# Kernel tuning notes

Hardware: AMD Instinct MI355X
Metric: run time of the kernel (lower is better)

Reference implementation:

```python
import jax, jax.numpy as jnp
import numpy as np
import math

B, L, D_IN = 4, 8192, 64
H = 256          # d_model
N2 = 32          # d_state // 2 complex conjugate pairs (S4D)
NL = 4           # n_layers
D_OUT = 10


def setup_inputs() -> dict:
    key = jax.random.key(0)
    ks = jax.random.split(key, 16)
    x = jax.random.normal(ks[0], (B, L, D_IN), dtype=jnp.float32)
    # encoder Linear(d_input, d_model)
    enc_W = jax.random.normal(ks[1], (H, D_IN), dtype=jnp.float32) / np.sqrt(D_IN)
    enc_b = jnp.zeros((H,), dtype=jnp.float32)
    # per-layer S4D parameters (stacked over n_layers)
    log_dt = jax.random.uniform(ks[2], (NL, H), dtype=jnp.float32,
                                minval=math.log(1e-3), maxval=math.log(1e-1))
    log_A_re = jnp.full((NL, H, N2), math.log(0.5), dtype=jnp.float32)
    A_im = jnp.tile(math.pi * jnp.arange(N2, dtype=jnp.float32), (NL, H, 1))
    C_re = jax.random.normal(ks[3], (NL, H, N2), dtype=jnp.float32) * (0.5 ** 0.5)
    C_im = jax.random.normal(ks[4], (NL, H, N2), dtype=jnp.float32) * (0.5 ** 0.5)
    D = jax.random.normal(ks[5], (NL, H), dtype=jnp.float32)
    # S4 block output linear (H -> 2H) followed by GLU
    Wo = jax.random.normal(ks[6], (NL, 2 * H, H), dtype=jnp.float32) / np.sqrt(H)
    bo = jnp.zeros((NL, 2 * H), dtype=jnp.float32)
    # post-norm LayerNorm over d_model
    ln_w = jnp.ones((NL, H), dtype=jnp.float32)
    ln_b = jnp.zeros((NL, H), dtype=jnp.float32)
    # final decoder Linear(d_model, d_output)
    out_W = jax.random.normal(ks[7], (D_OUT, H), dtype=jnp.float32) / np.sqrt(H)
    out_b = jnp.zeros((D_OUT,), dtype=jnp.float32)
    return dict(x=x, enc_W=enc_W, enc_b=enc_b, log_dt=log_dt, log_A_re=log_A_re,
                A_im=A_im, C_re=C_re, C_im=C_im, D=D, Wo=Wo, bo=bo,
                ln_w=ln_w, ln_b=ln_b, out_W=out_W, out_b=out_b)


def _s4d_kernel(log_dt, log_A_re, A_im, C_re, C_im, L):
    # S4D-ZOH-ish (S4D-Lin) kernel: K[h,l] = 2 Re sum_n C~[h,n] exp(l*dt*A[h,n])
    dt = jnp.exp(log_dt)[:, None]                      # (H,1)
    A = -jnp.exp(log_A_re) + 1j * A_im                 # (H,N2)
    dtA = dt * A                                       # (H,N2)
    Ct = (C_re + 1j * C_im) * (jnp.exp(dtA) - 1.0) / A # (H,N2)
    t = jnp.arange(L, dtype=jnp.float32)
    V = jnp.exp(dtA[:, :, None] * t)                   # (H,N2,L) Vandermonde
    return 2.0 * jnp.einsum('hn,hnl->hl', Ct, V).real  # (H,L)


def reference(x, enc_W, enc_b, log_dt, log_A_re, A_im, C_re, C_im, D, Wo, bo,
              ln_w, ln_b, out_W, out_b):
    Bc, Lc, _ = x.shape
    h = x @ enc_W.T + enc_b          # (B,L,H)
    h = h.transpose(0, 2, 1)         # (B,H,L) (transposed layout)
    n_layers = log_dt.shape[0]
    for i in range(n_layers):
        K = _s4d_kernel(log_dt[i], log_A_re[i], A_im[i], C_re[i], C_im[i], Lc)
        # FFT convolution (causal, non-circular via 2L padding)
        Kf = jnp.fft.rfft(K, n=2 * Lc)                       # (H, L+1)
        hf = jnp.fft.rfft(h, n=2 * Lc)                       # (B,H,L+1)
        y = jnp.fft.irfft(hf * Kf, n=2 * Lc)[..., :Lc]
        y = y + D[i][:, None] * h                            # skip D*u
        y = jax.nn.gelu(y)
        # output linear (H -> 2H) + GLU, pointwise over length
        u = jnp.einsum('oh,bhl->bol', Wo[i], y) + bo[i][:, None]
        Hd = h.shape[1]
        z = u[:, :Hd] * jax.nn.sigmoid(u[:, Hd:])
        h = z + h                                            # residual
        # post-norm LayerNorm over channel (d_model) dim
        mu = h.mean(axis=1, keepdims=True)
        var = h.var(axis=1, keepdims=True)
        h = (h - mu) / jnp.sqrt(var + 1e-5) * ln_w[i][:, None] + ln_b[i][:, None]
    h = h.transpose(0, 2, 1)          # (B,L,H)
    return h @ out_W.T + out_b        # (B,L,d_output)
```

## Files before the change

### kernel.cpp

```cpp
#include <hip/hip_runtime.h>
#include <hip/hip_bf16.h>


constexpr int B_ = 4, L_ = 8192, DIN = 64, H_ = 256, N2_ = 32, NL_ = 4, DOUT = 10;
constexpr int LC = 64, CHK = L_ / LC;
constexpr int GCH = B_ * CHK;
constexpr int M_ = B_ * L_;

constexpr size_t OFF_H    = 0;
constexpr size_t OFF_WOB  = 8388608;
constexpr size_t OFF_PW   = 8650752;
constexpr size_t OFF_PCT  = 8716288;
constexpr size_t OFF_PWLC = 8781824;
constexpr size_t OFF_PZ   = 8847360;
constexpr size_t OFF_EWT  = 8912896;
constexpr size_t OFF_UCM  = 8929280;
constexpr size_t OFF_YCM  = 13123584;
constexpr size_t OFF_MT   = 21512192;
constexpr size_t OFF_MW   = 22036480;
constexpr size_t OFF_MV   = 22560768;

typedef short bf16x8 __attribute__((ext_vector_type(8)));
typedef short short8 __attribute__((ext_vector_type(8)));
typedef float f32x4  __attribute__((ext_vector_type(4)));
typedef int   int2v  __attribute__((ext_vector_type(2)));

__device__ __forceinline__ float b2f(short s) {
    union { float f; unsigned u; } c;
    c.u = ((unsigned)(unsigned short)s) << 16;
    return c.f;
}

__global__ __launch_bounds__(256) void k_params(
    const float* __restrict__ log_dt, const float* __restrict__ log_A_re,
    const float* __restrict__ A_im, const float* __restrict__ C_re,
    const float* __restrict__ C_im, float* __restrict__ ws)
{
    int idx = blockIdx.x * 256 + threadIdx.x;
    if (idx >= NL_ * H_ * N2_) return;
    int i  = idx / (H_ * N2_);
    int hh = (idx / N2_) % H_;
    float dt  = expf(log_dt[i * H_ + hh]);
    float Are = -expf(log_A_re[idx]);
    float Aim = A_im[idx];
    float zre = dt * Are, zim = dt * Aim;
    float er  = expf(zre);
    float wre = er * cosf(zim), wim = er * sinf(zim);
    float d   = Are * Are + Aim * Aim;
    float nre = wre - 1.f, nim = wim;
    float qre = (nre * Are + nim * Aim) / d;
    float qim = (nim * Are - nre * Aim) / d;
    float cr = C_re[idx], ci = C_im[idx];
    float ctre = cr * qre - ci * qim;
    float ctim = cr * qim + ci * qre;
    float er2 = expf(zre * (float)LC);
    float wlre = er2 * cosf(zim * (float)LC);
    float wlim = er2 * sinf(zim * (float)LC);
    ((float2*)(ws + OFF_PW))[idx]   = make_float2(wre, wim);
    ((float2*)(ws + OFF_PCT))[idx]  = make_float2(2.f * ctre, 2.f * ctim);
    ((float2*)(ws + OFF_PWLC))[idx] = make_float2(wlre, wlim);
    ((float2*)(ws + OFF_PZ))[idx]   = make_float2(zre, zim);
}

__global__ __launch_bounds__(256) void k_mats(const float* __restrict__ ws,
    int layer, __hip_bfloat16* __restrict__ mt, __hip_bfloat16* __restrict__ mw,
    __hip_bfloat16* __restrict__ mv)
{
    int h = blockIdx.x, tid = threadIdx.x;
    __shared__ float zre[32], zim[32], ctr[32], cti[32], kv[64];
    if (tid < 32) {
        float2 z = ((const float2*)(ws + OFF_PZ))[(size_t)layer*H_*N2_ + h*N2_ + tid];
        float2 c = ((const float2*)(ws + OFF_PCT))[(size_t)layer*H_*N2_ + h*N2_ + tid];
        zre[tid] = z.x; zim[tid] = z.y; ctr[tid] = c.x; cti[tid] = c.y;
    }
    __syncthreads();
    if (tid < 64) {
        float d = (float)tid, acc = 0.f;
        for (int n = 0; n < 32; n++) {
            float er = expf(zre[n] * d);
            float co = cosf(zim[n] * d), si = sinf(zim[n] * d);
            acc += er * (ctr[n] * co - cti[n] * si);
        }
        kv[tid] = acc;
    }
    __syncthreads();
    {
        int t = tid >> 2, j0 = (tid & 3) * 16;
        alignas(16) __hip_bfloat16 row[16];
        #pragma unroll
        for (int jj = 0; jj < 16; jj++) {
            int j = j0 + jj;
            row[jj] = __float2bfloat16(j <= t ? kv[t - j] : 0.f);
        }
        *(short8*)(mt + (size_t)h*4096 + t*64 + j0)     = *(short8*)&row[0];
        *(short8*)(mt + (size_t)h*4096 + t*64 + j0 + 8) = *(short8*)&row[8];
    }
    {
        int n = tid >> 3, j0 = (tid & 7) * 8;
        alignas(16) __hip_bfloat16 rre[8], rim[8];
        #pragma unroll
        for (int jj = 0; jj < 8; jj++) {
            float e = (float)(63 - (j0 + jj));
            float er = expf(zre[n] * e);
            rre[jj] = __float2bfloat16(er * cosf(zim[n] * e));
            rim[jj] = __float2bfloat16(er * sinf(zim[n] * e));
        }
        *(short8*)(mw + (size_t)h*4096 + (2*n)*64 + j0)   = *(short8*)&rre[0];
        *(short8*)(mw + (size_t)h*4096 + (2*n+1)*64 + j0) = *(short8*)&rim[0];
    }
    {
        int t = tid >> 2, n0 = (tid & 3) * 8;
        float e = (float)(t + 1);
        alignas(16) __hip_bfloat16 row[16];
        #pragma unroll
        for (int k = 0; k < 8; k++) {
            int n = n0 + k;
            float er = expf(zre[n] * e);
            float wr = er * cosf(zim[n] * e), wi = er * sinf(zim[n] * e);
            row[2*k]   = __float2bfloat16(ctr[n]*wr - cti[n]*wi);
            row[2*k+1] = __float2bfloat16(-(ctr[n]*wi + cti[n]*wr));
        }
        *(short8*)(mv + (size_t)h*4096 + t*64 + 2*n0)     = *(short8*)&row[0];
        *(short8*)(mv + (size_t)h*4096 + t*64 + 2*n0 + 8) = *(short8*)&row[8];
    }
}

__global__ __launch_bounds__(256) void k_transpose(const float* __restrict__ src,
    float* __restrict__ dst, int R, int Cc)
{
    __shared__ float t[32][33];
    int x = blockIdx.x * 32 + threadIdx.x;
    #pragma unroll
    for (int i = 0; i < 4; i++) {
        int yy = blockIdx.y * 32 + threadIdx.y + i * 8;
        if (x < Cc && yy < R) t[threadIdx.y + i * 8][threadIdx.x] = src[(size_t)yy * Cc + x];
    }
    __syncthreads();
    int xo = blockIdx.y * 32 + threadIdx.x;
    #pragma unroll
    for (int i = 0; i < 4; i++) {
        int yo = blockIdx.x * 32 + threadIdx.y + i * 8;
        if (xo < R && yo < Cc) dst[(size_t)yo * R + xo] = t[threadIdx.x][threadIdx.y + i * 8];
    }
}

__global__ __launch_bounds__(256) void k_wcvt(const float* __restrict__ src,
    __hip_bfloat16* __restrict__ dst, int n4)
{
    int i = blockIdx.x * 256 + threadIdx.x;
    if (i >= n4) return;
    float4 v = ((const float4*)src)[i];
    union { __hip_bfloat16 b[4]; uint2 u; } o;
    o.b[0] = __float2bfloat16(v.x); o.b[1] = __float2bfloat16(v.y);
    o.b[2] = __float2bfloat16(v.z); o.b[3] = __float2bfloat16(v.w);
    ((uint2*)dst)[i] = o.u;
}

__global__ __launch_bounds__(256) void k_encoder(const float* __restrict__ x,
    const float* __restrict__ encWT, const float* __restrict__ enc_b,
    __hip_bfloat16* __restrict__ hfr, __hip_bfloat16* __restrict__ ucm)
{
    __shared__ float As[DIN][36];
    __shared__ float Bs[32][268];
    int m0e = blockIdx.x * 32;
    int tid = threadIdx.x;
    const float4* x4 = (const float4*)x;
    #pragma unroll
    for (int q = 0; q < 2; q++) {
        int f = tid * 2 + q;
        int row = f >> 4, kq = f & 15;
        float4 v = x4[(size_t)(m0e + row) * 16 + kq];
        As[kq * 4 + 0][row] = v.x; As[kq * 4 + 1][row] = v.y;
        As[kq * 4 + 2][row] = v.z; As[kq * 4 + 3][row] = v.w;
    }
    int tx = tid & 31, ty = tid >> 5;
    float acc[4][8];
    #pragma unroll
    for (int p = 0; p < 4; p++)
        #pragma unroll
        for (int j = 0; j < 8; j++) acc[p][j] = 0.f;
    const float4* w4 = (const float4*)encWT;
    for (int ks = 0; ks < 2; ks++) {
        __syncthreads();
        #pragma unroll
        for (int it = 0; it < 8; it++) {
            int q = it * 256 + tid;
            int row = q >> 6, c4 = q & 63;
            *(float4*)&Bs[row][c4 * 4] = w4[ks * 2048 + q];
        }
        __syncthreads();
        #pragma unroll 8
        for (int kk = 0; kk < 32; kk++) {
            int k = ks * 32 + kk;
            float4 a  = *(const float4*)&As[k][ty * 4];
            float4 b0 = *(const float4*)&Bs[kk][tx * 4];
            float4 b1 = *(const float4*)&Bs[kk][128 + tx * 4];
            float av[4] = {a.x, a.y, a.z, a.w};
            float bv[8] = {b0.x, b0.y, b0.z, b0.w, b1.x, b1.y, b1.z, b1.w};
            #pragma unroll
            for (int p = 0; p < 4; p++)
                #pragma unroll
                for (int j = 0; j < 8; j++)
                    acc[p][j] = fmaf(av[p], bv[j], acc[p][j]);
        }
    }
    float4 eb0 = *(const float4*)&enc_b[tx * 4];
    float4 eb1 = *(const float4*)&enc_b[128 + tx * 4];
    float ebv[8] = {eb0.x, eb0.y, eb0.z, eb0.w, eb1.x, eb1.y, eb1.z, eb1.w};
    __syncthreads();
    #pragma unroll
    for (int p = 0; p < 4; p++) {
        int pl = ty * 4 + p;
        #pragma unroll
        for (int j = 0; j < 4; j++) Bs[pl][tx * 4 + j]       = acc[p][j] + ebv[j];
        #pragma unroll
        for (int j = 0; j < 4; j++) Bs[pl][128 + tx * 4 + j] = acc[p][j + 4] + ebv[j + 4];
    }
    __syncthreads();
    {
        size_t m0 = (size_t)(m0e & ~63);
        int mi = (m0e >> 5) & 1;
        int nq = tid >> 6, l = tid & 63, l4 = l >> 4, l15 = l & 15;
        int tid32 = (mi * 4 + nq) * 64 + l;
        __hip_bfloat16* dst = hfr + m0 * 256 + (size_t)tid32 * 32;
        alignas(16) __hip_bfloat16 tmp[32];
        #pragma unroll
        for (int sub = 0; sub < 2; sub++)
            #pragma unroll
            for (int nj = 0; nj < 4; nj++) {
                int pl = sub * 16 + l4 * 4;
                int cn = nq * 64 + nj * 16 + l15;
                #pragma unroll
                for (int r = 0; r < 4; r++)
                    tmp[sub * 16 + nj * 4 + r] = __float2bfloat16(Bs[pl + r][cn]);
            }
        #pragma unroll
        for (int q = 0; q < 4; q++)
            *(short8*)(dst + q * 8) = *(short8*)&tmp[q * 8];
    }
    {
        alignas(16) __hip_bfloat16 row[32];
        #pragma unroll
        for (int pl = 0; pl < 32; pl++) row[pl] = __float2bfloat16(Bs[pl][tid]);
        #pragma unroll
        for (int q = 0; q < 4; q++)
            *(short8*)(ucm + (size_t)tid * M_ + m0e + q * 8) = *(short8*)&row[q * 8];
    }
}

__global__ __launch_bounds__(256) void k_ssm(const __hip_bfloat16* __restrict__ ucm,
    const __hip_bfloat16* __restrict__ mt, const __hip_bfloat16* __restrict__ mw,
    const __hip_bfloat16* __restrict__ mv, const float* __restrict__ ws, int layer,
    const float* __restrict__ Dp, __hip_bfloat16* __restrict__ ycm)
{
    __shared__ __hip_bfloat16 ulds[L_];
    __shared__ __hip_bfloat16 st[CHK * 64];
    __shared__ float segT[8][32][2];
    int h = blockIdx.x >> 2, b = blockIdx.x & 3;
    int tid = threadIdx.x, w = tid >> 6, l = tid & 63, l15 = l & 15, l4 = l >> 4;
    const __hip_bfloat16* ub = ucm + (size_t)h * M_ + (size_t)b * L_;
    #pragma unroll
    for (int it = 0; it < 4; it++) {
        int e0 = it * 2048 + tid * 8;
        short8 v = *(const short8*)(ub + e0);
        int c = e0 >> 6, e = e0 & 63;
        *(short8*)&ulds[c * 64 + (e ^ ((c & 7) << 3))] = v;
    }
    __syncthreads();
    {
        const __hip_bfloat16* bbase = mw + (size_t)h * 4096 + l15 * 64 + l4 * 8;
        #pragma unroll
        for (int half = 0; half < 2; half++) {
            int g0 = (w + half * 4) * 16;
            int ca = g0 + l15;
            f32x4 acc[4];
            #pragma unroll
            for (int nj = 0; nj < 4; nj++) acc[nj] = (f32x4)0.f;
            #pragma unroll
            for (int ks = 0; ks < 2; ks++) {
                int e = l4 * 8 + ks * 32;
                bf16x8 a = *(const bf16x8*)&ulds[ca * 64 + (e ^ ((ca & 7) << 3))];
                #pragma unroll
                for (int nj = 0; nj < 4; nj++) {
                    bf16x8 bb = *(const bf16x8*)(bbase + nj * 16 * 64 + ks * 32);
                    acc[nj] = __builtin_amdgcn_mfma_f32_16x16x32_bf16(a, bb, acc[nj], 0, 0, 0);
                }
            }
            #pragma unroll
            for (int nj = 0; nj < 4; nj++)
                #pragma unroll
                for (int r = 0; r < 4; r++) {
                    int c = g0 + l4 * 4 + r, e = nj * 16 + l15;
                    st[c * 64 + (e ^ ((c & 7) << 3))] = __float2bfloat16(acc[nj][r]);
                }
        }
    }
    __syncthreads();
    {
        int s = tid >> 5, n = tid & 31;
        float2 wl = ((const float2*)(ws + OFF_PWLC))[(size_t)layer * H_ * N2_ + h * 32 + n];
        float tr = 0.f, ti = 0.f;
        for (int j = 0; j < 16; j++) {
            int c = s * 16 + j;
            __hip_bfloat162* p = (__hip_bfloat162*)&st[c * 64 + ((2 * n) ^ ((c & 7) << 3))];
            float2 v = __bfloat1622float2(*p);
            float nr = fmaf(wl.x, tr, v.x); nr = fmaf(-wl.y, ti, nr);
            float ni = fmaf(wl.x, ti, v.y); ni = fmaf(wl.y, tr, ni);
            tr = nr; ti = ni;
        }
        segT[s][n][0] = tr; segT[s][n][1] = ti;
        __syncthreads();
        float wr = wl.x, wi = wl.y;
        #pragma unroll
        for (int q = 0; q < 4; q++) {
            float nr = wr * wr - wi * wi, ni = 2.f * wr * wi;
            wr = nr; wi = ni;
        }
        float ar = 0.f, ai = 0.f;
        for (int t = 0; t < s; t++) {
            float Tx = segT[t][n][0], Ty = segT[t][n][1];
            float nr = fmaf(wr, ar, Tx); nr = fmaf(-wi, ai, nr);
            float ni = fmaf(wr, ai, Ty); ni = fmaf(wi, ar, ni);
            ar = nr; ai = ni;
        }
        for (int j = 0; j < 16; j++) {
            int c = s * 16 + j;
            __hip_bfloat162* p = (__hip_bfloat162*)&st[c * 64 + ((2 * n) ^ ((c & 7) << 3))];
            float2 v = __bfloat1622float2(*p);
            *p = __float22bfloat162_rn(make_float2(ar, ai));
            float nr = fmaf(wl.x, ar, v.x); nr = fmaf(-wl.y, ai, nr);
            float ni = fmaf(wl.x, ai, v.y); ni = fmaf(wl.y, ar, ni);
            ar = nr; ai = ni;
        }
    }
    __syncthreads();
    {
        const __hip_bfloat16* bt = mt + (size_t)h * 4096 + l15 * 64 + l4 * 8;
        const __hip_bfloat16* bv = mv + (size_t)h * 4096 + l15 * 64 + l4 * 8;
        float Dh = Dp[layer * H_ + h];
        __hip_bfloat16* yb = ycm + (size_t)h * M_ + (size_t)b * L_;
        #pragma unroll
        for (int half = 0; half < 2; half++) {
            int g0 = (w + half * 4) * 16;
            int ca = g0 + l15;
            f32x4 acc[4];
            #pragma unroll
            for (int nj = 0; nj < 4; nj++) acc[nj] = (f32x4)0.f;
            #pragma unroll
            for (int ks = 0; ks < 2; ks++) {
                int e = l4 * 8 + ks * 32;
                bf16x8 a = *(const bf16x8*)&ulds[ca * 64 + (e ^ ((ca & 7) << 3))];
                #pragma unroll
                for (int nj = 0; nj < 4; nj++) {
                    bf16x8 bb = *(const bf16x8*)(bt + nj * 16 * 64 + ks * 32);
                    acc[nj] = __builtin_amdgcn_mfma_f32_16x16x32_bf16(a, bb, acc[nj], 0, 0, 0);
                }
            }
            #pragma unroll
            for (int ks = 0; ks < 2; ks++) {
                int e = l4 * 8 + ks * 32;
                bf16x8 a = *(const bf16x8*)&st[ca * 64 + (e ^ ((ca & 7) << 3))];
                #pragma unroll
                for (int nj = 0; nj < 4; nj++) {
                    bf16x8 bb = *(const bf16x8*)(bv + nj * 16 * 64 + ks * 32);
                    acc[nj] = __builtin_amdgcn_mfma_f32_16x16x32_bf16(a, bb, acc[nj], 0, 0, 0);
                }
            }
            #pragma unroll
            for (int nj = 0; nj < 4; nj++)
                #pragma unroll
                for (int r = 0; r < 4; r++) {
                    int g = g0 + l4 * 4 + r;
                    int e = nj * 16 + l15;
                    float uv = __bfloat162float(ulds[g * 64 + (e ^ ((g & 7) << 3))]);
                    float v = fmaf(Dh, uv, acc[nj][r]);
                    float gg = 0.7978845608028654f * fmaf(0.044715f * v, v * v, v);
                    float yv = v / (1.f + __expf(-2.f * gg));
                    yb[(size_t)g * 64 + nj * 16 + l15] = __float2bfloat16(yv);
                }
        }
    }
}

__global__ __launch_bounds__(256) void k_glu_mfma(
    const __hip_bfloat16* __restrict__ ycm,
    __hip_bfloat16* __restrict__ hfr,
    const __hip_bfloat16* __restrict__ wob,
    const float* __restrict__ bo, const float* __restrict__ lnw,
    const float* __restrict__ lnb, __hip_bfloat16* __restrict__ un)
{
    __shared__ int buf[4352];
    __shared__ float red[4][32][2];
    int tid = threadIdx.x;
    int w = tid >> 6, l = tid & 63, l15 = l & 15, l4 = l >> 4;
    int m0 = blockIdx.x * 32;
    int mi = (m0 >> 5) & 1;
    int nv = w * 64;

    {
        int p = tid & 127, ph = tid >> 7;
        const __hip_bfloat16* s0 = ycm + (size_t)(2 * p) * M_ + m0 + ph * 16;
        const __hip_bfloat16* s1 = s0 + M_;
        short8 y0a = *(const short8*)(s0);
        short8 y0b = *(const short8*)(s0 + 8);
        short8 y1a = *(const short8*)(s1);
        short8 y1b = *(const short8*)(s1 + 8);
        int* dst = buf + ph * 16 * 130 + p;
        #pragma unroll
        for (int j = 0; j < 8; j++) {
            dst[j * 130] = ((int)(unsigned short)y0a[j]) | (((int)(unsigned short)y1a[j]) << 16);
            dst[(8 + j) * 130] = ((int)(unsigned short)y0b[j]) | (((int)(unsigned short)y1b[j]) << 16);
        }
    }
    __hip_bfloat16* hbase = hfr + (size_t)(m0 & ~63) * 256
                            + ((size_t)((mi * 4 + w) * 64 + l)) * 32;
    bf16x8 hraw[4];
    #pragma unroll
    for (int q = 0; q < 4; q++) hraw[q] = *(const bf16x8*)(hbase + q * 8);
    __syncthreads();

    f32x4 accv[2][4], accg[2][4];
    #pragma unroll
    for (int sub = 0; sub < 2; sub++)
        #pragma unroll
        for (int nj = 0; nj < 4; nj++) { accv[sub][nj] = (f32x4)0.f; accg[sub][nj] = (f32x4)0.f; }

    int abase0 = l15 * 130 + l4 * 4;
    #pragma unroll 2
    for (int ks = 0; ks < 8; ks++) {
        int k0 = ks * 32 + l4 * 8;
        union { int2v d[2]; bf16x8 v; } a0u, a1u;
        a0u.d[0] = *(const int2v*)&buf[abase0 + ks * 16];
        a0u.d[1] = *(const int2v*)&buf[abase0 + ks * 16 + 2];
        a1u.d[0] = *(const int2v*)&buf[abase0 + 16 * 130 + ks * 16];
        a1u.d[1] = *(const int2v*)&buf[abase0 + 16 * 130 + ks * 16 + 2];
        bf16x8 a0 = a0u.v;
        bf16x8 a1 = a1u.v;
        #pragma unroll
        for (int nj = 0; nj < 4; nj++) {
            bf16x8 bv = *(const bf16x8*)(wob + (size_t)(nv + nj * 16 + l15) * H_ + k0);
            bf16x8 bg = *(const bf16x8*)(wob + (size_t)(256 + nv + nj * 16 + l15) * H_ + k0);
            accv[0][nj] = __builtin_amdgcn_mfma_f32_16x16x32_bf16(a0, bv, accv[0][nj], 0, 0, 0);
            accg[0][nj] = __builtin_amdgcn_mfma_f32_16x16x32_bf16(a0, bg, accg[0][nj], 0, 0, 0);
            accv[1][nj] = __builtin_amdgcn_mfma_f32_16x16x32_bf16(a1, bv, accv[1][nj], 0, 0, 0);
            accg[1][nj] = __builtin_amdgcn_mfma_f32_16x16x32_bf16(a1, bg, accg[1][nj], 0, 0, 0);
        }
    }

    float bov[4], bog[4], lw[4], lb[4];
    #pragma unroll
    for (int nj = 0; nj < 4; nj++) {
        int cn = nv + nj * 16 + l15;
        bov[nj] = bo[cn]; bog[nj] = bo[256 + cn];
        lw[nj] = lnw[cn]; lb[nj] = lnb[cn];
    }
    #pragma unroll
    for (int sub = 0; sub < 2; sub++) {
        #pragma unroll
        for (int r = 0; r < 4; r++) {
            int lr = sub * 16 + l4 * 4 + r;
            float s = 0.f, ss = 0.f;
            #pragma unroll
            for (int nj = 0; nj < 4; nj++) {
                int idx = sub * 16 + nj * 4 + r;
                float uv = accv[sub][nj][r] + bov[nj];
                float ug = accg[sub][nj][r] + bog[nj];
                float z = uv / (1.f + __expf(-ug));
                float v = z + b2f(hraw[idx >> 3][idx & 7]);
                accv[sub][nj][r] = v;
                s += v; ss += v * v;
            }
            #pragma unroll
            for (int off = 1; off < 16; off <<= 1) {
                s  += __shfl_xor(s, off);
                ss += __shfl_xor(ss, off);
            }
            if (l15 == 0) { red[w][lr][0] = s; red[w][lr][1] = ss; }
        }
    }
    __syncthreads();
    short* lt = (short*)buf;
    alignas(16) __hip_bfloat16 tmp[32];
    #pragma unroll
    for (int sub = 0; sub < 2; sub++) {
        #pragma unroll
        for (int r = 0; r < 4; r++) {
            int lr = sub * 16 + l4 * 4 + r;
            float s  = red[0][lr][0] + red[1][lr][0] + red[2][lr][0] + red[3][lr][0];
            float ss = red[0][lr][1] + red[1][lr][1] + red[2][lr][1] + red[3][lr][1];
            float mu = s * (1.f / 256.f);
            float var = ss * (1.f / 256.f) - mu * mu;
            float rstd = rsqrtf(var + 1e-5f);
            #pragma unroll
            for (int nj = 0; nj < 4; nj++) {
                int cn = nv + nj * 16 + l15;
                int idx = sub * 16 + nj * 4 + r;
                float val = (accv[sub][nj][r] - mu) * rstd * lw[nj] + lb[nj];
                __hip_bfloat16 bval = __float2bfloat16(val);
                tmp[idx] = bval;
                lt[cn * 34 + lr] = *(short*)&bval;
            }
        }
    }
    #pragma unroll
    for (int q = 0; q < 4; q++)
        *(short8*)(hbase + q * 8) = *(short8*)&tmp[q * 8];
    __syncthreads();
    {
        #pragma unroll
        for (int q = 0; q < 4; q++)
            *(short8*)(un + (size_t)tid * M_ + m0 + q * 8)
                = *(short8*)&lt[tid * 34 + q * 8];
    }
}

__global__ __launch_bounds__(256) void k_decoder(const __hip_bfloat16* __restrict__ hfr,
    const float* __restrict__ out_W, const float* __restrict__ out_b,
    float* __restrict__ out)
{
    __shared__ float hs[64][260];
    __shared__ float wl[10][260];
    int m0 = blockIdx.x * 64;
    int tid = threadIdx.x;
    #pragma unroll
    for (int half = 0; half < 2; half++) {
        int cid = half * 256 + tid;
        int cw = cid >> 6, cl = cid & 63;
        int cmi = cw >> 2, cnq = cw & 3, cl4 = cl >> 4, cl15 = cl & 15;
        const bf16x8* src = (const bf16x8*)(hfr + (size_t)m0 * 256 + (size_t)cid * 32);
        bf16x8 raw[4];
        #pragma unroll
        for (int q = 0; q < 4; q++) raw[q] = src[q];
        #pragma unroll
        for (int sub = 0; sub < 2; sub++)
            #pragma unroll
            for (int nj = 0; nj < 4; nj++) {
                int row = cmi * 32 + sub * 16 + cl4 * 4;
                int col = cnq * 64 + nj * 16 + cl15;
                #pragma unroll
                for (int r = 0; r < 4; r++) {
                    int idx = sub * 16 + nj * 4 + r;
                    hs[row + r][col] = b2f(raw[idx >> 3][idx & 7]);
                }
            }
    }
    for (int q = tid; q < 640; q += 256) {
        int r = q / 64, k4 = q % 64;
        *(float4*)&wl[r][k4 * 4] = ((const float4*)out_W)[q];
    }
    __syncthreads();
    int slot = tid & 15;
    if (slot < DOUT) {
        #pragma unroll
        for (int pass = 0; pass < 4; pass++) {
            int pl = pass * 16 + (tid >> 4);
            float a0 = 0.f, a1 = 0.f, a2 = 0.f, a3 = 0.f;
            #pragma unroll 8
            for (int k = 0; k < 256; k += 4) {
                a0 = fmaf(hs[pl][k + 0], wl[slot][k + 0], a0);
                a1 = fmaf(hs[pl][k + 1], wl[slot][k + 1], a1);
                a2 = fmaf(hs[pl][k + 2], wl[slot][k + 2], a2);
                a3 = fmaf(hs[pl][k + 3], wl[slot][k + 3], a3);
            }
            out[(size_t)(m0 + pl) * DOUT + slot] = (a0 + a1) + (a2 + a3) + out_b[slot];
        }
    }
}

extern "C" void kernel_launch(void* const* d_in, const int* in_sizes, int n_in,
                              void* d_out, int out_size, void* d_ws, size_t ws_size,
                              hipStream_t stream)
{
    (void)in_sizes; (void)n_in; (void)out_size; (void)ws_size;
    const float* x        = (const float*)d_in[0];
    const float* enc_W    = (const float*)d_in[1];
    const float* enc_b    = (const float*)d_in[2];
    const float* log_dt   = (const float*)d_in[3];
    const float* log_A_re = (const float*)d_in[4];
    const float* A_im     = (const float*)d_in[5];
    const float* C_re     = (const float*)d_in[6];
    const float* C_im     = (const float*)d_in[7];
    const float* Dp       = (const float*)d_in[8];
    const float* Wo       = (const float*)d_in[9];
    const float* bo       = (const float*)d_in[10];
    const float* lnw      = (const float*)d_in[11];
    const float* lnb      = (const float*)d_in[12];
    const float* out_W    = (const float*)d_in[13];
    const float* out_b    = (const float*)d_in[14];
    float* ws = (float*)d_ws;
    __hip_bfloat16* hfr = (__hip_bfloat16*)(ws + OFF_H);
    __hip_bfloat16* ucm = (__hip_bfloat16*)(ws + OFF_UCM);
    __hip_bfloat16* ycm = (__hip_bfloat16*)(ws + OFF_YCM);
    __hip_bfloat16* mt = (__hip_bfloat16*)(ws + OFF_MT);
    __hip_bfloat16* mw = (__hip_bfloat16*)(ws + OFF_MW);
    __hip_bfloat16* mv = (__hip_bfloat16*)(ws + OFF_MV);
    __hip_bfloat16* wob = (__hip_bfloat16*)(ws + OFF_WOB);

    k_params<<<NL_ * H_ * N2_ / 256, 256, 0, stream>>>(log_dt, log_A_re, A_im, C_re, C_im, ws);
    dim3 tb(32, 8);
    k_transpose<<<dim3(DIN / 32, H_ / 32), tb, 0, stream>>>(enc_W, ws + OFF_EWT, H_, DIN);
    k_wcvt<<<(NL_ * 2 * H_ * H_ / 4 + 255) / 256, 256, 0, stream>>>(Wo, wob, NL_ * 2 * H_ * H_ / 4);
    k_encoder<<<M_ / 32, 256, 0, stream>>>(x, ws + OFF_EWT, enc_b, hfr, ucm);
    for (int i = 0; i < NL_; i++) {
        k_mats<<<H_, 256, 0, stream>>>(ws, i, mt, mw, mv);
        k_ssm<<<H_ * B_, 256, 0, stream>>>(ucm, mt, mw, mv, ws, i, Dp, ycm);
        k_glu_mfma<<<M_ / 32, 256, 0, stream>>>(ycm, hfr,
            wob + (size_t)i * 2 * H_ * H_, bo + (size_t)i * 2 * H_,
            lnw + (size_t)i * H_, lnb + (size_t)i * H_, ucm);
    }
    k_decoder<<<M_ / 64, 256, 0, stream>>>(hfr, out_W, out_b, (float*)d_out);
}
```

Baseline: 441.8 us.

## Drop duplicate fragment-layout hidden state; read residual from channel-major buffer

The hidden state was kept in two copies: a row-major MFMA-fragment layout (hfr) and a channel-major copy (ucm). This change removes hfr. The encoder and GLU kernels now write only the channel-major buffer. The GLU kernel stages the residual from that buffer through shared memory, and the decoder reads it directly. This removes one full-size hidden-state write and read per layer, at the cost of doubling the GLU kernel's shared memory (which may lower occupancy) and a transposed residual read from LDS.

```diff
diff --git a/kernel.cpp b/kernel.cpp
--- a/kernel.cpp
+++ b/kernel.cpp
@@ -7,7 +7,6 @@
 constexpr int GCH = B_ * CHK;
 constexpr int M_ = B_ * L_;
 
-constexpr size_t OFF_H    = 0;
 constexpr size_t OFF_WOB  = 8388608;
 constexpr size_t OFF_PW   = 8650752;
 constexpr size_t OFF_PCT  = 8716288;
@@ -158,7 +157,7 @@
 
 __global__ __launch_bounds__(256) void k_encoder(const float* __restrict__ x,
     const float* __restrict__ encWT, const float* __restrict__ enc_b,
-    __hip_bfloat16* __restrict__ hfr, __hip_bfloat16* __restrict__ ucm)
+    __hip_bfloat16* __restrict__ u)
 {
     __shared__ float As[DIN][36];
     __shared__ float Bs[32][268];
@@ -218,33 +217,12 @@
     }
     __syncthreads();
     {
-        size_t m0 = (size_t)(m0e & ~63);
-        int mi = (m0e >> 5) & 1;
-        int nq = tid >> 6, l = tid & 63, l4 = l >> 4, l15 = l & 15;
-        int tid32 = (mi * 4 + nq) * 64 + l;
-        __hip_bfloat16* dst = hfr + m0 * 256 + (size_t)tid32 * 32;
-        alignas(16) __hip_bfloat16 tmp[32];
-        #pragma unroll
-        for (int sub = 0; sub < 2; sub++)
-            #pragma unroll
-            for (int nj = 0; nj < 4; nj++) {
-                int pl = sub * 16 + l4 * 4;
-                int cn = nq * 64 + nj * 16 + l15;
-                #pragma unroll
-                for (int r = 0; r < 4; r++)
-                    tmp[sub * 16 + nj * 4 + r] = __float2bfloat16(Bs[pl + r][cn]);
-            }
+        alignas(16) __hip_bfloat16 row[32];
+        #pragma unroll
+        for (int pl = 0; pl < 32; pl++) row[pl] = __float2bfloat16(Bs[pl][tid]);
         #pragma unroll
         for (int q = 0; q < 4; q++)
-            *(short8*)(dst + q * 8) = *(short8*)&tmp[q * 8];
-    }
-    {
-        alignas(16) __hip_bfloat16 row[32];
-        #pragma unroll
-        for (int pl = 0; pl < 32; pl++) row[pl] = __float2bfloat16(Bs[pl][tid]);
-        #pragma unroll
-        for (int q = 0; q < 4; q++)
-            *(short8*)(ucm + (size_t)tid * M_ + m0e + q * 8) = *(short8*)&row[q * 8];
+            *(short8*)(u + (size_t)tid * M_ + m0e + q * 8) = *(short8*)&row[q * 8];
     }
 }
 
@@ -384,39 +362,44 @@
 
 __global__ __launch_bounds__(256) void k_glu_mfma(
     const __hip_bfloat16* __restrict__ ycm,
-    __hip_bfloat16* __restrict__ hfr,
     const __hip_bfloat16* __restrict__ wob,
     const float* __restrict__ bo, const float* __restrict__ lnw,
-    const float* __restrict__ lnb, __hip_bfloat16* __restrict__ un)
-{
-    __shared__ int buf[4352];
+    const float* __restrict__ lnb,
+    __hip_bfloat16* __restrict__ u)
+{
+    __shared__ int buf[8320];
     __shared__ float red[4][32][2];
+    int* bufA = buf;
+    int* bufR = buf + 4160;
     int tid = threadIdx.x;
     int w = tid >> 6, l = tid & 63, l15 = l & 15, l4 = l >> 4;
     int m0 = blockIdx.x * 32;
-    int mi = (m0 >> 5) & 1;
     int nv = w * 64;
 
     {
         int p = tid & 127, ph = tid >> 7;
-        const __hip_bfloat16* s0 = ycm + (size_t)(2 * p) * M_ + m0 + ph * 16;
-        const __hip_bfloat16* s1 = s0 + M_;
-        short8 y0a = *(const short8*)(s0);
-        short8 y0b = *(const short8*)(s0 + 8);
-        short8 y1a = *(const short8*)(s1);
-        short8 y1b = *(const short8*)(s1 + 8);
-        int* dst = buf + ph * 16 * 130 + p;
+        const __hip_bfloat16* a0p = ycm + (size_t)(2 * p) * M_ + m0 + ph * 16;
+        const __hip_bfloat16* a1p = a0p + M_;
+        const __hip_bfloat16* r0p = u + (size_t)(2 * p) * M_ + m0 + ph * 16;
+        const __hip_bfloat16* r1p = r0p + M_;
+        short8 a0a = *(const short8*)(a0p);
+        short8 a0b = *(const short8*)(a0p + 8);
+        short8 a1a = *(const short8*)(a1p);
+        short8 a1b = *(const short8*)(a1p + 8);
+        short8 r0a = *(const short8*)(r0p);
+        short8 r0b = *(const short8*)(r0p + 8);
+        short8 r1a = *(const short8*)(r1p);
+        short8 r1b = *(const short8*)(r1p + 8);
+        int* da = bufA + ph * 16 * 130 + p;
+        int* dr = bufR + ph * 16 * 130 + p;
         #pragma unroll
         for (int j = 0; j < 8; j++) {
-            dst[j * 130] = ((int)(unsigned short)y0a[j]) | (((int)(unsigned short)y1a[j]) << 16);
-            dst[(8 + j) * 130] = ((int)(unsigned short)y0b[j]) | (((int)(unsigned short)y1b[j]) << 16);
-        }
-    }
-    __hip_bfloat16* hbase = hfr + (size_t)(m0 & ~63) * 256
-                            + ((size_t)((mi * 4 + w) * 64 + l)) * 32;
-    bf16x8 hraw[4];
-    #pragma unroll
-    for (int q = 0; q < 4; q++) hraw[q] = *(const bf16x8*)(hbase + q * 8);
+            da[j * 130]       = ((int)(unsigned short)a0a[j]) | (((int)(unsigned short)a1a[j]) << 16);
+            da[(8 + j) * 130] = ((int)(unsigned short)a0b[j]) | (((int)(unsigned short)a1b[j]) << 16);
+            dr[j * 130]       = ((int)(unsigned short)r0a[j]) | (((int)(unsigned short)r1a[j]) << 16);
+            dr[(8 + j) * 130] = ((int)(unsigned short)r0b[j]) | (((int)(unsigned short)r1b[j]) << 16);
+        }
+    }
     __syncthreads();
 
     f32x4 accv[2][4], accg[2][4];
@@ -430,10 +413,10 @@
     for (int ks = 0; ks < 8; ks++) {
         int k0 = ks * 32 + l4 * 8;
         union { int2v d[2]; bf16x8 v; } a0u, a1u;
-        a0u.d[0] = *(const int2v*)&buf[abase0 + ks * 16];
-        a0u.d[1] = *(const int2v*)&buf[abase0 + ks * 16 + 2];
-        a1u.d[0] = *(const int2v*)&buf[abase0 + 16 * 130 + ks * 16];
-        a1u.d[1] = *(const int2v*)&buf[abase0 + 16 * 130 + ks * 16 + 2];
+        a0u.d[0] = *(const int2v*)&bufA[abase0 + ks * 16];
+        a0u.d[1] = *(const int2v*)&bufA[abase0 + ks * 16 + 2];
+        a1u.d[0] = *(const int2v*)&bufA[abase0 + 16 * 130 + ks * 16];
+        a1u.d[1] = *(const int2v*)&bufA[abase0 + 16 * 130 + ks * 16 + 2];
         bf16x8 a0 = a0u.v;
         bf16x8 a1 = a1u.v;
         #pragma unroll
@@ -454,6 +437,7 @@
         bov[nj] = bo[cn]; bog[nj] = bo[256 + cn];
         lw[nj] = lnw[cn]; lb[nj] = lnb[cn];
     }
+    const short* bufRs = (const short*)bufR;
     #pragma unroll
     for (int sub = 0; sub < 2; sub++) {
         #pragma unroll
@@ -462,11 +446,11 @@
             float s = 0.f, ss = 0.f;
             #pragma unroll
             for (int nj = 0; nj < 4; nj++) {
-                int idx = sub * 16 + nj * 4 + r;
+                int cn = nv + nj * 16 + l15;
                 float uv = accv[sub][nj][r] + bov[nj];
                 float ug = accg[sub][nj][r] + bog[nj];
                 float z = uv / (1.f + __expf(-ug));
-                float v = z + b2f(hraw[idx >> 3][idx & 7]);
+                float v = z + b2f(bufRs[lr * 260 + cn]);
                 accv[sub][nj][r] = v;
                 s += v; ss += v * v;
             }
@@ -480,7 +464,6 @@
     }
     __syncthreads();
     short* lt = (short*)buf;
-    alignas(16) __hip_bfloat16 tmp[32];
     #pragma unroll
     for (int sub = 0; sub < 2; sub++) {
         #pragma unroll
@@ -494,27 +477,22 @@
             #pragma unroll
             for (int nj = 0; nj < 4; nj++) {
                 int cn = nv + nj * 16 + l15;
-                int idx = sub * 16 + nj * 4 + r;
                 float val = (accv[sub][nj][r] - mu) * rstd * lw[nj] + lb[nj];
                 __hip_bfloat16 bval = __float2bfloat16(val);
-                tmp[idx] = bval;
                 lt[cn * 34 + lr] = *(short*)&bval;
             }
         }
     }
-    #pragma unroll
-    for (int q = 0; q < 4; q++)
-        *(short8*)(hbase + q * 8) = *(short8*)&tmp[q * 8];
     __syncthreads();
     {
         #pragma unroll
         for (int q = 0; q < 4; q++)
-            *(short8*)(un + (size_t)tid * M_ + m0 + q * 8)
+            *(short8*)(u + (size_t)tid * M_ + m0 + q * 8)
                 = *(short8*)&lt[tid * 34 + q * 8];
     }
 }
 
-__global__ __launch_bounds__(256) void k_decoder(const __hip_bfloat16* __restrict__ hfr,
+__global__ __launch_bounds__(256) void k_decoder(const __hip_bfloat16* __restrict__ u,
     const float* __restrict__ out_W, const float* __restrict__ out_b,
     float* __restrict__ out)
 {
@@ -522,27 +500,14 @@
     __shared__ float wl[10][260];
     int m0 = blockIdx.x * 64;
     int tid = threadIdx.x;
-    #pragma unroll
-    for (int half = 0; half < 2; half++) {
-        int cid = half * 256 + tid;
-        int cw = cid >> 6, cl = cid & 63;
-        int cmi = cw >> 2, cnq = cw & 3, cl4 = cl >> 4, cl15 = cl & 15;
-        const bf16x8* src = (const bf16x8*)(hfr + (size_t)m0 * 256 + (size_t)cid * 32);
-        bf16x8 raw[4];
-        #pragma unroll
-        for (int q = 0; q < 4; q++) raw[q] = src[q];
-        #pragma unroll
-        for (int sub = 0; sub < 2; sub++)
-            #pragma unroll
-            for (int nj = 0; nj < 4; nj++) {
-                int row = cmi * 32 + sub * 16 + cl4 * 4;
-                int col = cnq * 64 + nj * 16 + cl15;
-                #pragma unroll
-                for (int r = 0; r < 4; r++) {
-                    int idx = sub * 16 + nj * 4 + r;
-                    hs[row + r][col] = b2f(raw[idx >> 3][idx & 7]);
-                }
-            }
+    {
+        const __hip_bfloat16* src = u + (size_t)tid * M_ + m0;
+        bf16x8 raw[8];
+        #pragma unroll
+        for (int q = 0; q < 8; q++) raw[q] = *(const bf16x8*)(src + q * 8);
+        #pragma unroll
+        for (int p = 0; p < 64; p++)
+            hs[p][tid] = b2f(raw[p >> 3][p & 7]);
     }
     for (int q = tid; q < 640; q += 256) {
         int r = q / 64, k4 = q % 64;
@@ -588,8 +553,7 @@
     const float* out_W    = (const float*)d_in[13];
     const float* out_b    = (const float*)d_in[14];
     float* ws = (float*)d_ws;
-    __hip_bfloat16* hfr = (__hip_bfloat16*)(ws + OFF_H);
-    __hip_bfloat16* ucm = (__hip_bfloat16*)(ws + OFF_UCM);
+    __hip_bfloat16* u   = (__hip_bfloat16*)(ws + OFF_UCM);
     __hip_bfloat16* ycm = (__hip_bfloat16*)(ws + OFF_YCM);
     __hip_bfloat16* mt = (__hip_bfloat16*)(ws + OFF_MT);
     __hip_bfloat16* mw = (__hip_bfloat16*)(ws + OFF_MW);
@@ -600,13 +564,13 @@
     dim3 tb(32, 8);
     k_transpose<<<dim3(DIN / 32, H_ / 32), tb, 0, stream>>>(enc_W, ws + OFF_EWT, H_, DIN);
     k_wcvt<<<(NL_ * 2 * H_ * H_ / 4 + 255) / 256, 256, 0, stream>>>(Wo, wob, NL_ * 2 * H_ * H_ / 4);
-    k_encoder<<<M_ / 32, 256, 0, stream>>>(x, ws + OFF_EWT, enc_b, hfr, ucm);
+    k_encoder<<<M_ / 32, 256, 0, stream>>>(x, ws + OFF_EWT, enc_b, u);
     for (int i = 0; i < NL_; i++) {
         k_mats<<<H_, 256, 0, stream>>>(ws, i, mt, mw, mv);
-        k_ssm<<<H_ * B_, 256, 0, stream>>>(ucm, mt, mw, mv, ws, i, Dp, ycm);
-        k_glu_mfma<<<M_ / 32, 256, 0, stream>>>(ycm, hfr,
+        k_ssm<<<H_ * B_, 256, 0, stream>>>(u, mt, mw, mv, ws, i, Dp, ycm);
+        k_glu_mfma<<<M_ / 32, 256, 0, stream>>>(ycm,
             wob + (size_t)i * 2 * H_ * H_, bo + (size_t)i * 2 * H_,
-            lnw + (size_t)i * H_, lnb + (size_t)i * H_, ucm);
-    }
-    k_decoder<<<M_ / 64, 256, 0, stream>>>(hfr, out_W, out_b, (float*)d_out);
-}
+            lnw + (size_t)i * H_, lnb + (size_t)i * H_, u);
+    }
+    k_decoder<<<M_ / 64, 256, 0, stream>>>(u, out_W, out_b, (float*)d_out);
+}
```

After: 449.1 us. About the same (+1.6%).
